# Optimization experiments

Measured on AMD Instinct MI355X. Metric: run time of the kernel, lower is better.

Reference implementation:

```python
import jax, jax.numpy as jnp
import numpy as np

B, S, D, H, E = 4, 2048, 512, 8, 4  # batch, seq, embed, heads, expand
HD = D // H


def setup_inputs() -> dict:
    key = jax.random.key(0)
    ks = jax.random.split(key, 9)
    s = lambda k, shape, fan: jax.random.normal(k, shape, jnp.float32) * (fan ** -0.5)
    return {
        "x": jax.random.normal(ks[0], (B, S, D), jnp.float32),
        "Wq": s(ks[1], (D, D), D),
        "Wk": s(ks[2], (D, D), D),
        "Wv": s(ks[3], (D, D), D),
        "Wo": s(ks[4], (D, D), D),
        "W1": s(ks[5], (D, D * E), D),
        "b1": jnp.zeros((D * E,), jnp.float32),
        "W2": s(ks[6], (D * E, D), D * E),
        "b2": jnp.zeros((D,), jnp.float32),
    }


def _encoder_layer(x, Wq, Wk, Wv, Wo, W1, b1, W2, b2):
    # NOTE: source computes InstanceNorm1d twice but discards both results -> no-ops.
    scale = D ** -0.25  # applied to BOTH q and k (net 1/sqrt(embed_dim))
    q = (x @ Wq).reshape(B, S, H, HD).transpose(0, 2, 1, 3) * scale  # [B,H,S,hd]
    k = (x @ Wk).reshape(B, S, H, HD).transpose(0, 2, 1, 3) * scale
    v = (x @ Wv).reshape(B, S, H, HD).transpose(0, 2, 1, 3)
    scores = jnp.einsum('bhqd,bhkd->bhqk', q, k)  # [B,H,S,S]
    attn = jax.nn.softmax(scores, axis=-1)
    o = jnp.einsum('bhqk,bhkd->bhqd', attn, v)  # [B,H,S,hd]
    o = o.transpose(0, 2, 1, 3).reshape(B, S, D)
    x = o @ Wo + x  # residual 1
    h = jax.nn.gelu(x @ W1 + b1, approximate=True)  # torch GELU(approximate='tanh')
    return h @ W2 + b2 + x  # residual 2 (dropout=0, eval)


def reference(x, Wq, Wk, Wv, Wo, W1, b1, W2, b2):
    return _encoder_layer(x, Wq, Wk, Wv, Wo, W1, b1, W2, b2)
```

## Files before the change

### kernel.cpp

```cpp
#include <hip/hip_runtime.h>
#include <hip/hip_bf16.h>


typedef __bf16 bf16;
typedef __attribute__((ext_vector_type(8))) __bf16 bf16x8;
typedef __attribute__((ext_vector_type(4))) __bf16 bf16x4;
typedef __attribute__((ext_vector_type(4))) float f32x4;
typedef __attribute__((ext_vector_type(16))) float f32x16;
typedef __attribute__((ext_vector_type(2))) unsigned int u32x2;
typedef __attribute__((ext_vector_type(4))) unsigned int u32x4;

#define LOG2E 1.4426950408889634f
#define SCORE_SCALE 0.044194173824159216f
#define SCALE_L2E (SCORE_SCALE * LOG2E)
#define FIXED_M 12.0f

#if __has_builtin(__builtin_amdgcn_exp2f)
#define EXP2(x) __builtin_amdgcn_exp2f(x)
#else
#define EXP2(x) exp2f(x)
#endif

__device__ __forceinline__ void gl_lds16(const bf16* g, bf16* l) {
  __builtin_amdgcn_global_load_lds(
      (const __attribute__((address_space(1))) unsigned int*)g,
      (__attribute__((address_space(3))) unsigned int*)l, 16, 0, 0);
}

template <int N>
__device__ __forceinline__ void wait_vm_barrier() {
  if constexpr (N == 0)
    asm volatile("s_waitcnt vmcnt(0)\ns_barrier" ::: "memory");
  else if constexpr (N == 3)
    asm volatile("s_waitcnt vmcnt(3)\ns_barrier" ::: "memory");
  else if constexpr (N == 4)
    asm volatile("s_waitcnt vmcnt(4)\ns_barrier" ::: "memory");
}

__device__ __forceinline__ float gelu_tanh(float x) {
  float u = 0.7978845608028654f * (x + 0.044715f * x * x * x);
  float e = EXP2(u * (2.0f * LOG2E));
  float th = 1.0f - 2.0f / (e + 1.0f);
  return 0.5f * x * (1.0f + th);
}

__device__ __forceinline__ f32x4 mfma_bf16(bf16x8 a, bf16x8 b, f32x4 c) {
  return __builtin_amdgcn_mfma_f32_16x16x32_bf16(a, b, c, 0, 0, 0);
}
__device__ __forceinline__ f32x16 mfma32x16(bf16x8 a, bf16x8 b, f32x16 c) {
  return __builtin_amdgcn_mfma_f32_32x32x16_bf16(a, b, c, 0, 0, 0);
}

__device__ __forceinline__ void plswap(unsigned int& a, unsigned int& b) {
  asm volatile("v_permlane32_swap_b32 %0, %1" : "+v"(a), "+v"(b));
}

template <int MODE, typename OutT, int TN>
__global__ __launch_bounds__(256, 2) void gemm_bt(
    const bf16* __restrict__ A, const bf16* __restrict__ Bt,
    OutT* __restrict__ C, const float* __restrict__ bias,
    const float* __restrict__ resf, const bf16* __restrict__ resb,
    bf16* __restrict__ vt, int M, int N, int K) {
  constexpr int MI = (TN == 128) ? 4 : 2;
  constexpr int NBUF = (TN == 128) ? 2 : 3;
  __shared__ __align__(16) bf16 sA[NBUF][128 * 32];
  __shared__ __align__(16) bf16 sB[NBUF][TN * 32];
  const int tid = threadIdx.x;
  const int lane = tid & 63;
  const int quad = lane >> 4, lc = lane & 15;
  const int wave = tid >> 6;
  const int wr = (TN == 128) ? (wave >> 1) : wave;
  const int wc = (TN == 128) ? (wave & 1) : 0;
  const int m0 = blockIdx.y * 128, n0 = blockIdx.x * TN;

  const int srow = tid >> 2;
  const int kc = (tid & 3) * 8;
  const bf16* Ag1 = A + (size_t)(m0 + srow) * K + kc;
  const bf16* Ag2 = A + (size_t)(m0 + 64 + srow) * K + kc;
  const bf16* Bg1 = Bt + (size_t)(n0 + srow) * K + kc;
  const bf16* Bg2 = Bt + (size_t)(n0 + 64 + srow) * K + kc;
  const int o1 = tid * 8, o2 = (tid + 256) * 8;

  f32x4 acc[MI][4];
#pragma unroll
  for (int mi = 0; mi < MI; ++mi)
#pragma unroll
    for (int ni = 0; ni < 4; ++ni) acc[mi][ni] = (f32x4){0.f, 0.f, 0.f, 0.f};

  const int kIters = K >> 5;

  if constexpr (TN == 128) {
    gl_lds16(Ag1, sA[0] + o1);
    gl_lds16(Ag2, sA[0] + o2);
    gl_lds16(Bg1, sB[0] + o1);
    gl_lds16(Bg2, sB[0] + o2);
    Ag1 += 32; Ag2 += 32; Bg1 += 32; Bg2 += 32;

    for (int kt = 0; kt < kIters; ++kt) {
      __syncthreads();
      const bf16* cA = sA[kt & 1];
      const bf16* cB = sB[kt & 1];
      if (kt + 1 < kIters) {
        bf16* nA = sA[(kt + 1) & 1];
        bf16* nB = sB[(kt + 1) & 1];
        gl_lds16(Ag1, nA + o1);
        gl_lds16(Ag2, nA + o2);
        gl_lds16(Bg1, nB + o1);
        gl_lds16(Bg2, nB + o2);
        Ag1 += 32; Ag2 += 32; Bg1 += 32; Bg2 += 32;
      }
      bf16x8 af[MI], bfm[4];
#pragma unroll
      for (int i = 0; i < MI; ++i)
        af[i] = *(const bf16x8*)(cA +
                                 ((wr * 64 + i * 16 + lc) * 32 + quad * 8));
#pragma unroll
      for (int i = 0; i < 4; ++i)
        bfm[i] =
            *(const bf16x8*)(cB + ((wc * 64 + i * 16 + lc) * 32 + quad * 8));
#pragma unroll
      for (int mi = 0; mi < MI; ++mi)
#pragma unroll
        for (int ni = 0; ni < 4; ++ni)
          acc[mi][ni] = mfma_bf16(af[mi], bfm[ni], acc[mi][ni]);
    }
  } else {
    auto stage = [&](int t) {
      bf16* a = sA[t % 3];
      bf16* bb = sB[t % 3];
      gl_lds16(Ag1 + t * 32, a + o1);
      gl_lds16(Ag2 + t * 32, a + o2);
      gl_lds16(Bg1 + t * 32, bb + o1);
    };
    stage(0);
    stage(1);
    for (int kt = 0; kt < kIters; ++kt) {
      if (kt + 1 < kIters)
        wait_vm_barrier<3>();
      else
        wait_vm_barrier<0>();
      if (kt + 2 < kIters) stage(kt + 2);
      const bf16* cA = sA[kt % 3];
      const bf16* cB = sB[kt % 3];
      bf16x8 af[MI], bfm[4];
#pragma unroll
      for (int i = 0; i < MI; ++i)
        af[i] = *(const bf16x8*)(cA +
                                 ((wr * 32 + i * 16 + lc) * 32 + quad * 8));
#pragma unroll
      for (int i = 0; i < 4; ++i)
        bfm[i] = *(const bf16x8*)(cB + ((i * 16 + lc) * 32 + quad * 8));
#pragma unroll
      for (int mi = 0; mi < MI; ++mi)
#pragma unroll
        for (int ni = 0; ni < 4; ++ni)
          acc[mi][ni] = mfma_bf16(af[mi], bfm[ni], acc[mi][ni]);
    }
  }

  if constexpr (MODE == 0) {
    if (n0 >= 1024) {
#pragma unroll
      for (int mi = 0; mi < MI; ++mi) {
        const int row0 = m0 + wr * (16 * MI) + mi * 16 + quad * 4;
        const int bb = row0 >> 11, s0 = row0 & 2047;
#pragma unroll
        for (int ni = 0; ni < 4; ++ni) {
          const int col = n0 + wc * 64 + ni * 16 + lc;
          const int hh = (col >> 6) & 7, d = col & 63;
          bf16x4 pb;
#pragma unroll
          for (int r = 0; r < 4; ++r) pb[r] = (bf16)acc[mi][ni][r];
          *(bf16x4*)(vt + ((size_t)((bb * 8 + hh) * 64 + d)) * 2048 + s0) = pb;
        }
      }
      return;
    }
  }
#pragma unroll
  for (int mi = 0; mi < MI; ++mi) {
#pragma unroll
    for (int r = 0; r < 4; ++r) {
      const int row = m0 + wr * (16 * MI) + mi * 16 + quad * 4 + r;
#pragma unroll
      for (int ni = 0; ni < 4; ++ni) {
        const int col = n0 + wc * 64 + ni * 16 + lc;
        const size_t idx = (size_t)row * N + col;
        float v = acc[mi][ni][r];
        if (MODE == 1) v += resf[idx];
        if (MODE == 2) v = gelu_tanh(v + bias[col]);
        if (MODE == 3) v += bias[col] + (float)resb[idx];
        C[idx] = (OutT)v;
      }
    }
  }
}

__global__ __launch_bounds__(512, 2) void gemm256(
    const bf16* __restrict__ A, const bf16* __restrict__ Bt,
    bf16* __restrict__ C, const float* __restrict__ bias, int M, int N,
    int K) {
  __shared__ __align__(16) bf16 sA[3][256 * 32];
  __shared__ __align__(16) bf16 sB[3][256 * 32];
  const int tid = threadIdx.x;
  const int lane = tid & 63;
  const int quad = lane >> 4, lc = lane & 15;
  const int w8 = tid >> 6;
  const int wr = w8 >> 2, wc = w8 & 3;
  const int m0 = blockIdx.y * 256, n0 = blockIdx.x * 256;

  const int sr = lane >> 2;
  const int sc = (lane & 3) * 8;

  f32x4 acc[8][4];
#pragma unroll
  for (int mi = 0; mi < 8; ++mi)
#pragma unroll
    for (int ni = 0; ni < 4; ++ni) acc[mi][ni] = (f32x4){0.f, 0.f, 0.f, 0.f};

  auto stage = [&](int t) {
    const int k0 = t * 32;
    bf16* a = sA[t % 3];
    bf16* bb = sB[t % 3];
#pragma unroll
    for (int j = 0; j < 2; ++j) {
      const int blk = w8 * 2 + j;
      gl_lds16(A + (size_t)(m0 + blk * 16 + sr) * K + k0 + sc, a + blk * 512);
      gl_lds16(Bt + (size_t)(n0 + blk * 16 + sr) * K + k0 + sc,
               bb + blk * 512);
    }
  };

  const int kIters = K >> 5;
  stage(0);
  stage(1);

  for (int kt = 0; kt < kIters; ++kt) {
    if (kt + 1 < kIters)
      wait_vm_barrier<4>();
    else
      wait_vm_barrier<0>();
    if (kt + 2 < kIters) stage(kt + 2);
    const bf16* cA = sA[kt % 3];
    const bf16* cB = sB[kt % 3];

    bf16x8 af[8], bfm[4];
#pragma unroll
    for (int i = 0; i < 8; ++i)
      af[i] =
          *(const bf16x8*)(cA + ((wr * 128 + i * 16 + lc) * 32 + quad * 8));
#pragma unroll
    for (int i = 0; i < 4; ++i)
      bfm[i] =
          *(const bf16x8*)(cB + ((wc * 64 + i * 16 + lc) * 32 + quad * 8));
#pragma unroll
    for (int mi = 0; mi < 8; ++mi)
#pragma unroll
      for (int ni = 0; ni < 4; ++ni)
        acc[mi][ni] = mfma_bf16(af[mi], bfm[ni], acc[mi][ni]);
  }

#pragma unroll
  for (int mi = 0; mi < 8; ++mi) {
#pragma unroll
    for (int r = 0; r < 4; ++r) {
      const int row = m0 + wr * 128 + mi * 16 + quad * 4 + r;
#pragma unroll
      for (int ni = 0; ni < 4; ++ni) {
        const int col = n0 + wc * 64 + ni * 16 + lc;
        C[(size_t)row * N + col] = (bf16)gelu_tanh(acc[mi][ni][r] + bias[col]);
      }
    }
  }
}

__global__ __launch_bounds__(256, 2) void flash_attn(
    const bf16* __restrict__ QKV, const bf16* __restrict__ Vt,
    bf16* __restrict__ O) {
  const int tid = threadIdx.x;
  const int lane = tid & 63, wave = tid >> 6;
  const int lo5 = lane & 31, hi = lane >> 5;
  const int lin = blockIdx.y * 16 + blockIdx.x;
  const int xcd = lin & 7, slot = lin >> 3;
  const int bh = xcd * 4 + (slot >> 4);
  const int qt = slot & 15;
  const int b = bh >> 3, h = bh & 7;
  const int q0 = qt * 128 + wave * 32;

  __shared__ __align__(16) bf16 sK[3][4096];
  __shared__ __align__(16) bf16 sV[3][4096];

  const bf16* Qrow = QKV + (size_t)(b * 2048 + q0 + lo5) * 1536 + h * 64;
  bf16x8 qf[4];
#pragma unroll
  for (int i = 0; i < 4; ++i) qf[i] = *(const bf16x8*)(Qrow + i * 16 + hi * 8);

  const int colsw = (((lane & 7) ^ (lane >> 3)) << 3);
  const bf16* Kg0 = QKV + (size_t)b * 2048 * 1536 + 512 + (size_t)h * 64 +
                    (size_t)(wave * 16 + (lane >> 3)) * 1536 + colsw;
  const bf16* Vg0 = Vt + (size_t)bh * 64 * 2048 +
                    (size_t)(wave * 16 + (lane >> 3)) * 2048 + colsw;
  const int stag = wave * 1024;
  const int m7 = lo5 & 7;

  f32x16 oacc[2];
  oacc[0] = (f32x16)(0.f);
  oacc[1] = (f32x16)(0.f);
  float rs0 = 0.f, rs1 = 0.f, rs2 = 0.f, rs3 = 0.f;

  auto stage = [&](int t) {
    bf16* dk = sK[t % 3] + stag;
    bf16* dv = sV[t % 3] + stag;
    gl_lds16(Kg0 + (size_t)t * 64 * 1536, dk);
    gl_lds16(Kg0 + (size_t)(t * 64 + 8) * 1536, dk + 512);
    gl_lds16(Vg0 + t * 64, dv);
    gl_lds16(Vg0 + t * 64 + 8 * 2048, dv + 512);
  };
  stage(0);
  stage(1);

  bf16x8 paw[4];

  auto softmax = [&](const f32x16& st, int hl) {
    unsigned int q32[4][2];
#pragma unroll
    for (int g = 0; g < 4; ++g) {
      bf16x4 pb;
      float p0 = EXP2(st[4 * g + 0] * SCALE_L2E - FIXED_M);
      float p1 = EXP2(st[4 * g + 1] * SCALE_L2E - FIXED_M);
      float p2 = EXP2(st[4 * g + 2] * SCALE_L2E - FIXED_M);
      float p3 = EXP2(st[4 * g + 3] * SCALE_L2E - FIXED_M);
      rs0 += p0; rs1 += p1; rs2 += p2; rs3 += p3;
      pb[0] = (bf16)p0; pb[1] = (bf16)p1; pb[2] = (bf16)p2; pb[3] = (bf16)p3;
      u32x2 w2 = __builtin_bit_cast(u32x2, pb);
      q32[g][0] = w2[0];
      q32[g][1] = w2[1];
    }
#pragma unroll
    for (int t = 0; t < 2; ++t) {
      unsigned int a0 = q32[2 * t][0], a1 = q32[2 * t][1];
      unsigned int b0 = q32[2 * t + 1][0], b1 = q32[2 * t + 1][1];
      plswap(a0, b0);
      plswap(a1, b1);
      u32x4 f = {a0, a1, b0, b1};
      paw[hl * 2 + t] = __builtin_bit_cast(bf16x8, f);
    }
  };

  for (int kt = 0; kt < 32; ++kt) {
    if (kt == 31)
      wait_vm_barrier<0>();
    else
      wait_vm_barrier<4>();
    if (kt + 2 < 32) stage(kt + 2);
    const bf16* cK = sK[kt % 3];
    const bf16* cV = sV[kt % 3];

    bf16x8 vf[2][4], kf[2][4];
#pragma unroll
    for (int dh = 0; dh < 2; ++dh) {
      const int Rd = dh * 32 + lo5;
#pragma unroll
      for (int w = 0; w < 4; ++w)
        vf[dh][w] =
            *(const bf16x8*)(cV + Rd * 64 + (((2 * w + hi) ^ m7) << 3));
    }
#pragma unroll
    for (int hl = 0; hl < 2; ++hl) {
      const int R = hl * 32 + lo5;
#pragma unroll
      for (int i = 0; i < 4; ++i)
        kf[hl][i] =
            *(const bf16x8*)(cK + R * 64 + (((2 * i + hi) ^ m7) << 3));
    }

    f32x16 st0 = (f32x16)(0.f), st1 = (f32x16)(0.f);
    __builtin_amdgcn_s_setprio(1);
#pragma unroll
    for (int i = 0; i < 4; ++i) {
      st0 = mfma32x16(kf[0][i], qf[i], st0);
      st1 = mfma32x16(kf[1][i], qf[i], st1);
    }
    __builtin_amdgcn_s_setprio(0);

    softmax(st0, 0);
#pragma unroll
    for (int w = 0; w < 2; ++w) {
      oacc[0] = mfma32x16(paw[w], vf[0][w], oacc[0]);
      oacc[1] = mfma32x16(paw[w], vf[1][w], oacc[1]);
    }
    softmax(st1, 1);
    __builtin_amdgcn_s_setprio(1);
#pragma unroll
    for (int w = 2; w < 4; ++w) {
      oacc[0] = mfma32x16(paw[w], vf[0][w], oacc[0]);
      oacc[1] = mfma32x16(paw[w], vf[1][w], oacc[1]);
    }
    __builtin_amdgcn_s_setprio(0);
  }

  float rsum = (rs0 + rs1) + (rs2 + rs3);
  rsum += __shfl_xor(rsum, 32, 64);
  const size_t obase = (size_t)(b * 2048 + q0) * 512 + h * 64;
#pragma unroll
  for (int r = 0; r < 16; ++r) {
    const int qloc = (r & 3) + 8 * (r >> 2) + 4 * hi;
    const float inv = 1.0f / __shfl(rsum, qloc, 64);
#pragma unroll
    for (int dh = 0; dh < 2; ++dh)
      O[obase + (size_t)qloc * 512 + dh * 32 + lo5] =
          (bf16)(oacc[dh][r] * inv);
  }
}

__global__ __launch_bounds__(256) void prep(
    const float* __restrict__ x, const float* __restrict__ Wq,
    const float* __restrict__ Wk, const float* __restrict__ Wv,
    const float* __restrict__ Wo, const float* __restrict__ W1,
    const float* __restrict__ W2, bf16* __restrict__ xb,
    bf16* __restrict__ WqkvT, bf16* __restrict__ WoT, bf16* __restrict__ W1T,
    bf16* __restrict__ W2T) {
  const int bid = blockIdx.x;
  if (bid < 4096) {
    const size_t i = ((size_t)bid * 256 + threadIdx.x) * 4;
    const float4 v = *(const float4*)(x + i);
    bf16x4 o;
    o[0] = (bf16)v.x; o[1] = (bf16)v.y; o[2] = (bf16)v.z; o[3] = (bf16)v.w;
    *(bf16x4*)(xb + i) = o;
    return;
  }
  const int t = bid - 4096;
  const float* in;
  bf16* out;
  int in_ld, out_ld, bx, by;
  if (t < 1024) {
    const int q = t >> 8, r = t & 255;
    bx = r & 15; by = r >> 4; in_ld = 512; out_ld = 512;
    in = (q == 0) ? Wq : (q == 1) ? Wk : (q == 2) ? Wv : Wo;
    out = (q == 0) ? WqkvT
          : (q == 1) ? WqkvT + 512 * 512
          : (q == 2) ? WqkvT + 2 * 512 * 512
                     : WoT;
  } else if (t < 2048) {
    const int r = t - 1024;
    bx = r & 63; by = r >> 6; in_ld = 2048; out_ld = 512;
    in = W1; out = W1T;
  } else {
    const int r = t - 2048;
    bx = r & 15; by = r >> 4; in_ld = 512; out_ld = 2048;
    in = W2; out = W2T;
  }
  __shared__ __align__(16) bf16 tl[32][33];
  const int tx = threadIdx.x & 31, ty = threadIdx.x >> 5;
  const int n0 = bx * 32, k0 = by * 32;
#pragma unroll
  for (int i = 0; i < 4; ++i)
    tl[ty + 8 * i][tx] = (bf16)in[(size_t)(k0 + ty + 8 * i) * in_ld + n0 + tx];
  __syncthreads();
#pragma unroll
  for (int i = 0; i < 4; ++i)
    out[(size_t)(n0 + ty + 8 * i) * out_ld + k0 + tx] = tl[tx][ty + 8 * i];
}

extern "C" void kernel_launch(void* const* d_in, const int* in_sizes, int n_in,
                              void* d_out, int out_size, void* d_ws,
                              size_t ws_size, hipStream_t stream) {
  const float* x = (const float*)d_in[0];
  const float* Wq = (const float*)d_in[1];
  const float* Wk = (const float*)d_in[2];
  const float* Wv = (const float*)d_in[3];
  const float* Wo = (const float*)d_in[4];
  const float* W1 = (const float*)d_in[5];
  const float* b1 = (const float*)d_in[6];
  const float* W2 = (const float*)d_in[7];
  const float* b2 = (const float*)d_in[8];
  float* out = (float*)d_out;

  char* ws = (char*)d_ws;
  size_t off = 0;
  auto alloc = [&](size_t bytes) {
    char* p = ws + off;
    off += (bytes + 255) & ~(size_t)255;
    return p;
  };
  bf16* WqkvT = (bf16*)alloc(1536ULL * 512 * 2);
  bf16* WoT = (bf16*)alloc(512ULL * 512 * 2);
  bf16* W1T = (bf16*)alloc(2048ULL * 512 * 2);
  bf16* W2T = (bf16*)alloc(512ULL * 2048 * 2);
  bf16* xb = (bf16*)alloc(8192ULL * 512 * 2);
  bf16* QKV = (bf16*)alloc(8192ULL * 1536 * 2);
  bf16* Vt = (bf16*)alloc(32ULL * 64 * 2048 * 2);
  bf16* attn = (bf16*)alloc(8192ULL * 512 * 2);
  bf16* x2 = xb;
  bf16* hbuf = QKV;

  const dim3 tb(256);
  prep<<<dim3(7168), tb, 0, stream>>>(x, Wq, Wk, Wv, Wo, W1, W2, xb, WqkvT,
                                      WoT, W1T, W2T);
  gemm_bt<0, bf16, 128><<<dim3(12, 64), tb, 0, stream>>>(
      xb, WqkvT, QKV, nullptr, nullptr, nullptr, Vt, 8192, 1536, 512);
  flash_attn<<<dim3(16, 32), tb, 0, stream>>>(QKV, Vt, attn);
  gemm_bt<1, bf16, 64><<<dim3(8, 64), tb, 0, stream>>>(
      attn, WoT, x2, nullptr, x, nullptr, nullptr, 8192, 512, 512);
  gemm256<<<dim3(8, 32), dim3(512), 0, stream>>>(x2, W1T, hbuf, b1, 8192,
                                                 2048, 512);
  gemm_bt<3, float, 64><<<dim3(8, 64), tb, 0, stream>>>(
      hbuf, W2T, out, b2, nullptr, x2, nullptr, 8192, 512, 2048);
}
```

Baseline: 251.7 us.

## Deepen W1 GEMM pipeline to 4 stages with swizzled LDS and split MFMA phases

The 256x256 W1 GEMM now keeps four LDS stages in flight instead of three, prefetching three K-tiles ahead. Staging uses an XOR swizzle on the 16-byte column chunk to cut LDS bank conflicts on fragment reads. The MFMA loop is split into two halves, each preceded by an extra barrier and run at raised wave priority, to interleave LDS reads with MFMA issue. This raises LDS use to 64KB per block and adds barriers, which could hurt occupancy at two blocks per CU.

```diff
diff --git a/kernel.cpp b/kernel.cpp
--- a/kernel.cpp
+++ b/kernel.cpp
@@ -35,6 +35,8 @@
     asm volatile("s_waitcnt vmcnt(3)\ns_barrier" ::: "memory");
   else if constexpr (N == 4)
     asm volatile("s_waitcnt vmcnt(4)\ns_barrier" ::: "memory");
+  else if constexpr (N == 8)
+    asm volatile("s_waitcnt vmcnt(8)\ns_barrier" ::: "memory");
 }
 
 __device__ __forceinline__ float gelu_tanh(float x) {
@@ -196,21 +198,21 @@
   }
 }
 
-__global__ __launch_bounds__(512, 2) void gemm256(
+__global__ __launch_bounds__(512, 2) void gemm256v2(
     const bf16* __restrict__ A, const bf16* __restrict__ Bt,
     bf16* __restrict__ C, const float* __restrict__ bias, int M, int N,
     int K) {
-  __shared__ __align__(16) bf16 sA[3][256 * 32];
-  __shared__ __align__(16) bf16 sB[3][256 * 32];
+  __shared__ __align__(16) bf16 sA[4][8192];
+  __shared__ __align__(16) bf16 sB[4][8192];
   const int tid = threadIdx.x;
   const int lane = tid & 63;
   const int quad = lane >> 4, lc = lane & 15;
   const int w8 = tid >> 6;
-  const int wr = w8 >> 2, wc = w8 & 3;
+  const int wm = w8 >> 2, wn = w8 & 3;
   const int m0 = blockIdx.y * 256, n0 = blockIdx.x * 256;
 
-  const int sr = lane >> 2;
-  const int sc = (lane & 3) * 8;
+  const int srow0 = tid >> 2;
+  const int cpos = tid & 3;
 
   f32x4 acc[8][4];
 #pragma unroll
@@ -219,55 +221,73 @@
     for (int ni = 0; ni < 4; ++ni) acc[mi][ni] = (f32x4){0.f, 0.f, 0.f, 0.f};
 
   auto stage = [&](int t) {
+    bf16* a = sA[t & 3];
+    bf16* bb = sB[t & 3];
     const int k0 = t * 32;
-    bf16* a = sA[t % 3];
-    bf16* bb = sB[t % 3];
-#pragma unroll
-    for (int j = 0; j < 2; ++j) {
-      const int blk = w8 * 2 + j;
-      gl_lds16(A + (size_t)(m0 + blk * 16 + sr) * K + k0 + sc, a + blk * 512);
-      gl_lds16(Bt + (size_t)(n0 + blk * 16 + sr) * K + k0 + sc,
-               bb + blk * 512);
+#pragma unroll
+    for (int c = 0; c < 2; ++c) {
+      const int row = c * 128 + srow0;
+      const int sc = (cpos ^ (row & 3)) * 8;
+      gl_lds16(A + (size_t)(m0 + row) * K + k0 + sc, a + c * 4096 + tid * 8);
+      gl_lds16(Bt + (size_t)(n0 + row) * K + k0 + sc, bb + c * 4096 + tid * 8);
     }
   };
 
   const int kIters = K >> 5;
   stage(0);
   stage(1);
+  stage(2);
+
+  const int cxq = (quad ^ (lc & 3)) << 3;
 
   for (int kt = 0; kt < kIters; ++kt) {
-    if (kt + 1 < kIters)
+    const int left = kIters - 1 - kt;
+    if (left >= 2)
+      wait_vm_barrier<8>();
+    else if (left == 1)
       wait_vm_barrier<4>();
     else
       wait_vm_barrier<0>();
-    if (kt + 2 < kIters) stage(kt + 2);
-    const bf16* cA = sA[kt % 3];
-    const bf16* cB = sB[kt % 3];
+    if (kt + 3 < kIters) stage(kt + 3);
+    const bf16* cA = sA[kt & 3];
+    const bf16* cB = sB[kt & 3];
 
     bf16x8 af[8], bfm[4];
 #pragma unroll
-    for (int i = 0; i < 8; ++i)
-      af[i] =
-          *(const bf16x8*)(cA + ((wr * 128 + i * 16 + lc) * 32 + quad * 8));
-#pragma unroll
     for (int i = 0; i < 4; ++i)
-      bfm[i] =
-          *(const bf16x8*)(cB + ((wc * 64 + i * 16 + lc) * 32 + quad * 8));
-#pragma unroll
-    for (int mi = 0; mi < 8; ++mi)
+      af[i] = *(const bf16x8*)(cA + (wm * 128 + i * 16 + lc) * 32 + cxq);
+#pragma unroll
+    for (int j = 0; j < 4; ++j)
+      bfm[j] = *(const bf16x8*)(cB + (wn * 64 + j * 16 + lc) * 32 + cxq);
+    __builtin_amdgcn_s_barrier();
+    __builtin_amdgcn_s_setprio(1);
+#pragma unroll
+    for (int mi = 0; mi < 4; ++mi)
 #pragma unroll
       for (int ni = 0; ni < 4; ++ni)
         acc[mi][ni] = mfma_bf16(af[mi], bfm[ni], acc[mi][ni]);
+    __builtin_amdgcn_s_setprio(0);
+#pragma unroll
+    for (int i = 4; i < 8; ++i)
+      af[i] = *(const bf16x8*)(cA + (wm * 128 + i * 16 + lc) * 32 + cxq);
+    __builtin_amdgcn_s_barrier();
+    __builtin_amdgcn_s_setprio(1);
+#pragma unroll
+    for (int mi = 4; mi < 8; ++mi)
+#pragma unroll
+      for (int ni = 0; ni < 4; ++ni)
+        acc[mi][ni] = mfma_bf16(af[mi], bfm[ni], acc[mi][ni]);
+    __builtin_amdgcn_s_setprio(0);
   }
 
 #pragma unroll
   for (int mi = 0; mi < 8; ++mi) {
 #pragma unroll
     for (int r = 0; r < 4; ++r) {
-      const int row = m0 + wr * 128 + mi * 16 + quad * 4 + r;
+      const int row = m0 + wm * 128 + mi * 16 + quad * 4 + r;
 #pragma unroll
       for (int ni = 0; ni < 4; ++ni) {
-        const int col = n0 + wc * 64 + ni * 16 + lc;
+        const int col = n0 + wn * 64 + ni * 16 + lc;
         C[(size_t)row * N + col] = (bf16)gelu_tanh(acc[mi][ni][r] + bias[col]);
       }
     }
@@ -502,8 +522,8 @@
   flash_attn<<<dim3(16, 32), tb, 0, stream>>>(QKV, Vt, attn);
   gemm_bt<1, bf16, 64><<<dim3(8, 64), tb, 0, stream>>>(
       attn, WoT, x2, nullptr, x, nullptr, nullptr, 8192, 512, 512);
-  gemm256<<<dim3(8, 32), dim3(512), 0, stream>>>(x2, W1T, hbuf, b1, 8192,
-                                                 2048, 512);
+  gemm256v2<<<dim3(8, 32), dim3(512), 0, stream>>>(x2, W1T, hbuf, b1, 8192,
+                                                   2048, 512);
   gemm_bt<3, float, 64><<<dim3(8, 64), tb, 0, stream>>>(
       hbuf, W2T, out, b2, nullptr, x2, nullptr, 8192, 512, 2048);
 }
```

Result: no change. 250.7 us (-0.4%).
